# Kernel optimization log

Hardware: AMD Instinct MI355X
Metric: run time of the kernel (lower is better)

Reference implementation:

```python
import jax, jax.numpy as jnp
import numpy as np
from jax import lax

K = 9  # propagation kernel

def conv(x, w, b, pad):
    y = lax.conv_general_dilated(x, w, (1, 1), [(pad, pad), (pad, pad)],
                                 dimension_numbers=('NCHW', 'OIHW', 'NCHW'))
    return y + b[None, :, None, None]

def bn(x, g, beta):
    # SynchronizedBatchNorm2d in eval mode with identity running stats (mean=0, var=1)
    return x * g[None, :, None, None] + beta[None, :, None, None]

def propagate(deep, wts):
    # Dynamic local filtering (same math as img2col * weights, sum over 81 taps),
    # computed as 81 shifted-slice FMAs instead of materializing the (n,c,hw,81) tensor.
    p = K // 2
    n, c, h, w = deep.shape
    padded = jnp.pad(deep, ((0, 0), (0, 0), (p, p), (p, p)))
    out = jnp.zeros_like(deep)
    for k in range(K * K):  # k = dy*9 + dx, matching unfold(2).unfold(3) flattening
        dy, dx = k // K, k % K
        out = out + padded[:, :, dy:dy + h, dx:dx + w] * wts[:, k:k + 1]
    return out

def setup_inputs():
    key = jax.random.key(0)
    ks = jax.random.split(key, 40)
    N, C, H, W = 1, 256, 96, 192
    NUM_CLASSES = 19
    s = 0.05
    f32 = jnp.float32
    d = {}
    d['f1_deep'] = jax.random.normal(ks[0], (N, C, H, W), f32)
    d['f1_low'] = jax.random.normal(ks[1], (N, C, H, W), f32)
    d['f2_low'] = jax.random.normal(ks[2], (N, C, H, W), f32)
    # WeightPredictor
    d['wp_c1_w'] = jax.random.normal(ks[3], (256, 256, 3, 3), f32) * s
    d['wp_c1_b'] = jnp.zeros((256,), f32)
    d['wp_c2_w'] = jax.random.normal(ks[4], (256, 512, 3, 3), f32) * s
    d['wp_c2_b'] = jnp.zeros((256,), f32)
    d['wp_fc_w'] = jax.random.normal(ks[5], (81, 256, 1, 1), f32) * s
    d['wp_fc_b'] = jnp.zeros((81,), f32)
    # AdaptiveScheduler
    d['sch_c1_w'] = jax.random.normal(ks[6], (256, 256, 3, 3), f32) * s
    d['sch_c1_b'] = jnp.zeros((256,), f32)
    d['sch_c2_w'] = jax.random.normal(ks[7], (256, 256, 3, 3), f32) * s
    d['sch_c2_b'] = jnp.zeros((256,), f32)
    d['sch_fc_w'] = jax.random.normal(ks[8], (1, 256), f32) * s
    d['sch_fc_b'] = jnp.zeros((1,), f32)
    # AdaptNet
    d['ad_c1_w'] = jax.random.normal(ks[9], (256, 512, 3, 3), f32) * s
    d['ad_c1_b'] = jnp.zeros((256,), f32)
    d['ad_c2_w'] = jax.random.normal(ks[10], (256, 256, 3, 3), f32) * s
    d['ad_c2_b'] = jnp.zeros((256,), f32)
    d['ad_c3_w'] = jax.random.normal(ks[11], (256, 256, 3, 3), f32) * s
    d['ad_c3_b'] = jnp.zeros((256,), f32)
    # reduce_conv2 (1x1 conv + BN)
    d['rc_w'] = jax.random.normal(ks[12], (48, 256, 1, 1), f32) * s
    d['rc_b'] = jnp.zeros((48,), f32)
    d['rc_g'] = jnp.ones((48,), f32)
    d['rc_beta'] = jnp.zeros((48,), f32)
    # last_conv
    d['lc1_w'] = jax.random.normal(ks[13], (256, 304, 3, 3), f32) * s
    d['lc1_b'] = jnp.zeros((256,), f32)
    d['lc1_g'] = jnp.ones((256,), f32)
    d['lc1_beta'] = jnp.zeros((256,), f32)
    d['lc2_w'] = jax.random.normal(ks[14], (256, 256, 3, 3), f32) * s
    d['lc2_b'] = jnp.zeros((256,), f32)
    d['lc2_g'] = jnp.ones((256,), f32)
    d['lc2_beta'] = jnp.zeros((256,), f32)
    d['lc3_w'] = jax.random.normal(ks[15], (NUM_CLASSES, 256, 1, 1), f32) * s
    d['lc3_b'] = jnp.zeros((NUM_CLASSES,), f32)
    return d

def reference(f1_deep, f1_low, f2_low,
              wp_c1_w, wp_c1_b, wp_c2_w, wp_c2_b, wp_fc_w, wp_fc_b,
              sch_c1_w, sch_c1_b, sch_c2_w, sch_c2_b, sch_fc_w, sch_fc_b,
              ad_c1_w, ad_c1_b, ad_c2_w, ad_c2_b, ad_c3_w, ad_c3_b,
              rc_w, rc_b, rc_g, rc_beta,
              lc1_w, lc1_b, lc1_g, lc1_beta,
              lc2_w, lc2_b, lc2_g, lc2_beta,
              lc3_w, lc3_b):
    n, c, h, w = f1_deep.shape
    # WeightPredictor: shared conv1 applied to both low features, cat, conv2, 1x1, softmax over 81 taps
    a1 = conv(f1_low, wp_c1_w, wp_c1_b, 1)
    a2 = conv(f2_low, wp_c1_w, wp_c1_b, 1)
    f = conv(jnp.concatenate([a1, a2], axis=1), wp_c2_w, wp_c2_b, 1)
    kernel = jax.nn.softmax(conv(f, wp_fc_w, wp_fc_b, 0), axis=1)  # (n,81,h,w)
    # AdaptiveScheduler
    diff = conv(f1_low, sch_c1_w, sch_c1_b, 1) - conv(f2_low, sch_c1_w, sch_c1_b, 1)
    o = conv(diff, sch_c2_w, sch_c2_b, 1)
    pooled = jnp.mean(o, axis=(2, 3)).squeeze()  # (256,) since n=1
    deviation = pooled @ sch_fc_w.T + sch_fc_b  # (1,)
    # PropagationModule (dynamic 9x9 local filtering of f1_deep by predicted per-pixel kernel)
    prop = propagate(f1_deep, kernel)  # (n,256,h,w)
    # AdaptNet
    x = conv(jnp.concatenate([f2_low, prop], axis=1), ad_c1_w, ad_c1_b, 1)
    x = conv(x, ad_c2_w, ad_c2_b, 1)
    x = conv(x, ad_c3_w, ad_c3_b, 1)
    # reduce_conv2 + last_conv
    low = bn(conv(f2_low, rc_w, rc_b, 0), rc_g, rc_beta)  # (n,48,h,w)
    x = jnp.concatenate([x, low], axis=1)  # (n,304,h,w)
    x = bn(conv(x, lc1_w, lc1_b, 1), lc1_g, lc1_beta)
    x = bn(conv(x, lc2_w, lc2_b, 1), lc2_g, lc2_beta)
    x = conv(x, lc3_w, lc3_b, 0)  # (n,19,h,w)
    out = jax.image.resize(x, (x.shape[0], x.shape[1], 4 * h, 4 * w), method='bilinear')
    return (out, deviation)
```

## Files before the change

kernel.cpp:

```cpp
#include <hip/hip_runtime.h>
#include <math.h>

#define HWIMG 18432
#define W2 194
#define H2 98
#define NPX1 (H2 * W2)
#define W4 200
#define H4 104
#define NPX4 (H4 * W4)
#define NOUT (19 * 384 * 768)

typedef short bf16x8 __attribute__((ext_vector_type(8)));
typedef float f32x4 __attribute__((ext_vector_type(4)));

__device__ __forceinline__ ushort bf16r(float f) {
    union { float f; unsigned u; } a; a.f = f;
    unsigned u = a.u;
    return (ushort)((u + 0x7fffu + ((u >> 16) & 1u)) >> 16);
}
__device__ __forceinline__ float b2f(ushort u) {
    union { unsigned i; float f; } a; a.i = ((unsigned)u) << 16;
    return a.f;
}
__device__ __forceinline__ bf16x8 ld8(const ushort* p) {
    return *reinterpret_cast<const bf16x8*>(p);
}

__device__ __forceinline__ void gld16(const ushort* g, ushort* l) {
    __builtin_amdgcn_global_load_lds(
        (const __attribute__((address_space(1))) unsigned int*)g,
        (__attribute__((address_space(3))) unsigned int*)l, 16, 0, 0);
}

#define MF16(a, b, c) __builtin_amdgcn_mfma_f32_16x16x32_bf16(a, b, c, 0, 0, 0)

__device__ __forceinline__ int swz(int L) { return L ^ (((L >> 7) & 7) << 4); }


__global__ __launch_bounds__(256) void xform_t_k(const float* __restrict__ src,
                                                 const float* __restrict__ src2,
                                                 ushort* __restrict__ dst)
{
    const int px = blockIdx.x * 32 + (threadIdx.x & 31);
    const int c8 = (blockIdx.y * 8 + (threadIdx.x >> 5)) * 8;
    if (px >= NPX1) return;
    const int yP = px / W2, xP = px % W2;
    const int y = yP - 1, x = xP - 1;
    ushort v[8];
    if (y >= 0 && y < 96 && x >= 0 && x < 192) {
        const int p = y * 192 + x;
#pragma unroll
        for (int j = 0; j < 8; ++j) {
            float f = src[(size_t)(c8 + j) * HWIMG + p];
            if (src2) f -= src2[(size_t)(c8 + j) * HWIMG + p];
            v[j] = bf16r(f);
        }
    } else {
#pragma unroll
        for (int j = 0; j < 8; ++j) v[j] = 0;
    }
    *reinterpret_cast<uint4*>(dst + ((size_t)(c8 >> 4) * NPX1 + px) * 16 + (c8 & 15))
        = *reinterpret_cast<uint4*>(v);
}

__global__ __launch_bounds__(256) void xform_nhwc_k(const float* __restrict__ src,
                                                    ushort* __restrict__ dst)
{
    const int px = blockIdx.x * 8 + (threadIdx.x >> 5);
    const int c8 = (threadIdx.x & 31) * 8;
    if (px >= NPX4) return;
    const int yP = px / W4, xP = px % W4;
    const int y = yP - 4, x = xP - 4;
    ushort v[8];
    if (y >= 0 && y < 96 && x >= 0 && x < 192) {
        const int p = y * 192 + x;
#pragma unroll
        for (int j = 0; j < 8; ++j) v[j] = bf16r(src[(size_t)(c8 + j) * HWIMG + p]);
    } else {
#pragma unroll
        for (int j = 0; j < 8; ++j) v[j] = 0;
    }
    *reinterpret_cast<uint4*>(dst + (size_t)px * 256 + c8) = *reinterpret_cast<uint4*>(v);
}

__global__ __launch_bounds__(256) void borderzero3_k(ushort* __restrict__ b0,
                                                     ushort* __restrict__ b1,
                                                     ushort* __restrict__ b2)
{
    ushort* buf = (blockIdx.y == 0) ? b0 : ((blockIdx.y == 1) ? b1 : b2);
    const int idx = blockIdx.x * 256 + threadIdx.x;
    if (idx >= 580 * 16) return;
    const int pi = idx % 580;
    const int cb = idx / 580;
    int pp;
    if (pi < 194) pp = pi;
    else if (pi < 388) pp = 97 * 194 + (pi - 194);
    else if (pi < 484) pp = (pi - 388 + 1) * 194;
    else pp = (pi - 484 + 1) * 194 + 193;
    uint4 z = {0, 0, 0, 0};
    ushort* p = buf + ((size_t)cb * NPX1 + pp) * 16;
    *reinterpret_cast<uint4*>(p) = z;
    *reinterpret_cast<uint4*>(p + 8) = z;
}

struct WtxJob {
    const float* w; const float* b; const float* g; const float* beta;
    int CoutR, Coutp, CinR0, kb0e, CinR1, KBt, ntaps, wtoff, biasoff;
};

__global__ __launch_bounds__(256) void wtx_multi_k(WtxJob J0, WtxJob J1, WtxJob J2,
                                                   WtxJob J3, WtxJob J4, WtxJob J5,
                                                   ushort* __restrict__ wt,
                                                   float* __restrict__ biasout)
{
    WtxJob J = J0;
    switch (blockIdx.y) {
        case 1: J = J1; break; case 2: J = J2; break; case 3: J = J3; break;
        case 4: J = J4; break; case 5: J = J5; break; default: break;
    }
    const int idx = blockIdx.x * 256 + threadIdx.x;
    const int total = J.ntaps * J.KBt * J.Coutp * 16;
    const int CinT = J.CinR0 + J.CinR1;
    if (idx < total) {
        const int c16 = idx & 15;
        const int oc = (idx >> 4) % J.Coutp;
        const int r2 = idx / (16 * J.Coutp);
        const int tap = r2 % J.ntaps;
        const int kbt = r2 / J.ntaps;
        const int k = kbt * 16 + c16;
        float val = 0.f;
        if (oc < J.CoutR) {
            int cit = -1;
            if (k < J.kb0e) { if (k < J.CinR0) cit = k; }
            else { const int k1 = k - J.kb0e; if (k1 < J.CinR1) cit = J.CinR0 + k1; }
            if (cit >= 0) {
                val = J.w[((size_t)oc * CinT + cit) * J.ntaps + tap];
                if (J.g) val *= J.g[oc];
            }
        }
        wt[J.wtoff + idx] = bf16r(val);
    } else if (idx < total + J.Coutp) {
        const int oc = idx - total;
        float v = 0.f;
        if (oc < J.CoutR) {
            v = J.b ? J.b[oc] : 0.f;
            if (J.g) v = v * J.g[oc] + J.beta[oc];
        }
        biasout[J.biasoff + oc] = v;
    }
}

struct ConvJob {
    const ushort* in0; const ushort* in1;
    int KB0, KB1;
    const ushort* wt;
    const float* bias;
    ushort* out;
    int CoutWr;
};

template<int NTAPS>
__device__ __forceinline__ void stage_kb(
    const ConvJob& J, int kb, int kbh, char* Ab, char* Bb,
    int y0, int x0, int ocb0, int Coutp, int tid, int b_r, int b_h8, int wu)
{
    constexpr int AROWS = (NTAPS == 9) ? 4 : 2;
    constexpr int AW = (NTAPS == 9) ? 66 : 64;
    constexpr int ASLOTS = AROWS * AW * 2;
    const ushort* plane = (kb < J.KB0)
        ? (J.in0 + (size_t)kb * (NPX1 * 16))
        : (J.in1 + (size_t)(kb - J.KB0) * (NPX1 * 16));
#pragma unroll
    for (int i = 0; i < (ASLOTS + 127) / 128; ++i) {
        const int f16 = i * 128 + tid;
        if ((ASLOTS % 128 == 0) || (f16 < ASLOTS)) {
            const int L = swz(f16 * 16);
            const int e = L >> 5;
            const int h8 = ((L >> 4) & 1) * 8;
            const int r = e / AW;
            const int xx = e - r * AW;
            const int px = (NTAPS == 9)
                ? (y0 - 1 + r) * W2 + (x0 - 1 + xx)
                : (y0 + r) * W2 + (x0 + xx);
            gld16(plane + (size_t)px * 16 + h8,
                  (ushort*)(Ab + __builtin_amdgcn_readfirstlane((f16 & ~63) * 16)));
        }
    }
    const ushort* wsrc = J.wt + ((size_t)kb * NTAPS * Coutp + ocb0 + b_r) * 16 + b_h8;
#pragma unroll
    for (int t = 0; t < NTAPS; ++t) {
        gld16(wsrc + (size_t)t * Coutp * 16, (ushort*)(Bb + (t * 2 + kbh) * 2048 + wu));
    }
}

template<int NTAPS>
__global__ __launch_bounds__(128) void conv_lds_k(ConvJob j0, ConvJob j1, ConvJob j2,
                                                  int Coutp)
{
    constexpr int AROWS = (NTAPS == 9) ? 4 : 2;
    constexpr int AW = (NTAPS == 9) ? 66 : 64;
    constexpr int APLANE = AROWS * AW * 32;
    __shared__ __align__(1024) char Abuf[2 * APLANE];
    __shared__ __align__(1024) char Bbuf[NTAPS * 2 * 2048];

    ConvJob J = j0;
    if (blockIdx.y == 1) J = j1;
    else if (blockIdx.y == 2) J = j2;

    const int nblk = gridDim.x;
    const int cpx = nblk >> 3;
    const int sw = ((int)blockIdx.x & 7) * cpx + ((int)blockIdx.x >> 3);
    const int pt = sw % 144;
    const int ocb0 = (sw / 144) * 64;
    const int y0 = (pt / 3) * 2 + 1;
    const int x0 = (pt % 3) * 64 + 1;

    const int tid = threadIdx.x;
    const int lane = tid & 63;
    const int wm = tid >> 6;
    const int l15 = lane & 15;
    const int kh16 = ((lane >> 4) & 1) * 16;
    const int pl = lane >> 5;

    const int bl = swz(tid * 16);
    const int b_r = bl >> 5;
    const int b_h8 = ((bl >> 4) & 1) * 8;
    const int wu = __builtin_amdgcn_readfirstlane((tid & ~63) * 16);

    const int KBtot = J.KB0 + J.KB1;

    f32x4 acc[4][4] = {};

    for (int s = 0; s < KBtot; s += 2) {
        stage_kb<NTAPS>(J, s,     0, Abuf,          Bbuf, y0, x0, ocb0, Coutp, tid, b_r, b_h8, wu);
        stage_kb<NTAPS>(J, s + 1, 1, Abuf + APLANE, Bbuf, y0, x0, ocb0, Coutp, tid, b_r, b_h8, wu);
        __syncthreads();

        const char* Ap = Abuf + pl * APLANE;
#pragma unroll
        for (int t = 0; t < NTAPS; ++t) {
            const int rowb = (NTAPS == 9) ? ((wm + t / 3) * AW + (t % 3)) : (wm * AW);
            const char* Bp = Bbuf + (t * 2 + pl) * 2048;
            bf16x8 a[4], b[4];
#pragma unroll
            for (int q = 0; q < 4; ++q) {
                const int la = (rowb + q * 16 + l15) * 32 + kh16;
                a[q] = ld8((const ushort*)(Ap + swz(la)));
                const int lb = (q * 16 + l15) * 32 + kh16;
                b[q] = ld8((const ushort*)(Bp + swz(lb)));
            }
#pragma unroll
            for (int i = 0; i < 4; ++i)
#pragma unroll
                for (int j = 0; j < 4; ++j)
                    acc[i][j] = MF16(a[i], b[j], acc[i][j]);
        }
        __syncthreads();
    }

    const int pxbase = (y0 + wm) * W2 + x0;
    const int r4 = (lane >> 4) * 4;
#pragma unroll
    for (int qo = 0; qo < 4; ++qo) {
        if (ocb0 + qo * 16 + 16 > J.CoutWr) continue;
        const int oc = ocb0 + qo * 16 + l15;
        const float bs = J.bias[oc];
        const size_t obase = (size_t)(oc >> 4) * ((size_t)NPX1 * 16) + (oc & 15);
#pragma unroll
        for (int qp = 0; qp < 4; ++qp) {
            const int pp = pxbase + qp * 16 + r4;
#pragma unroll
            for (int r = 0; r < 4; ++r)
                J.out[obase + (size_t)(pp + r) * 16] = bf16r(acc[qp][qo][r] + bs);
        }
    }
}

__global__ __launch_bounds__(256) void softmax81_k(ushort* __restrict__ t)
{
    const int p = blockIdx.x * 256 + threadIdx.x;
    if (p >= HWIMG) return;
    const int y = p / 192, x = p % 192;
    const size_t pp = (size_t)(y + 1) * W2 + (x + 1);
    float v[81];
    float m = -1e30f;
#pragma unroll
    for (int k = 0; k < 81; ++k) {
        v[k] = b2f(t[((size_t)(k >> 4) * NPX1 + pp) * 16 + (k & 15)]);
        m = fmaxf(m, v[k]);
    }
    float s = 0.f;
#pragma unroll
    for (int k = 0; k < 81; ++k) { v[k] = __expf(v[k] - m); s += v[k]; }
    const float inv = 1.f / s;
#pragma unroll
    for (int k = 0; k < 81; ++k)
        t[((size_t)(k >> 4) * NPX1 + pp) * 16 + (k & 15)] = bf16r(v[k] * inv);
}

__global__ __launch_bounds__(256) void prop_k(const ushort* __restrict__ deep,
                                              const ushort* __restrict__ ker,
                                              ushort* __restrict__ out)
{
    __shared__ float kl[8][81];
    const int pxb = blockIdx.x * 8;
    const int t = threadIdx.x;
    for (int i = t; i < 8 * 81; i += 256) {
        const int pp = pxb + i / 81, k = i % 81;
        float kv = 0.f;
        if (pp < NPX1) {
            const int yP = pp / W2, xP = pp % W2;
            if (yP >= 1 && yP <= 96 && xP >= 1 && xP <= 192)
                kv = b2f(ker[((size_t)(k >> 4) * NPX1 + pp) * 16 + (k & 15)]);
        }
        kl[i / 81][k] = kv;
    }
    __syncthreads();
    const int pi = t >> 5;
    const int c8 = (t & 31) * 8;
    const int pp = pxb + pi;
    if (pp >= NPX1) return;
    const int yP = pp / W2, xP = pp % W2;
    ushort* op = out + ((size_t)(c8 >> 4) * NPX1 + pp) * 16 + (c8 & 15);
    if (yP < 1 || yP > 96 || xP < 1 || xP > 192) {
        uint4 z = {0, 0, 0, 0};
        *reinterpret_cast<uint4*>(op) = z;
        return;
    }
    const int y = yP - 1, x = xP - 1;
    float acc[8];
#pragma unroll
    for (int j = 0; j < 8; ++j) acc[j] = 0.f;
    const ushort* dbase = deep + ((size_t)(y + 4) * W4 + (x + 4)) * 256 + c8;
#pragma unroll
    for (int k = 0; k < 81; ++k) {
        const int dy = k / 9 - 4, dx = k % 9 - 4;
        const float kv = kl[pi][k];
        bf16x8 d = ld8(dbase + (ptrdiff_t)(dy * W4 + dx) * 256);
#pragma unroll
        for (int j = 0; j < 8; ++j) acc[j] += b2f((ushort)d[j]) * kv;
    }
    ushort v[8];
#pragma unroll
    for (int j = 0; j < 8; ++j) v[j] = bf16r(acc[j]);
    *reinterpret_cast<uint4*>(op) = *reinterpret_cast<uint4*>(v);
}

__global__ __launch_bounds__(256) void rowsum_k(const ushort* __restrict__ t,
                                                float* __restrict__ partial)
{
    const int y = blockIdx.x >> 2;
    const int bx = blockIdx.x & 3;
    const int c = threadIdx.x;
    const size_t base = ((size_t)(c >> 4) * NPX1 + (size_t)(y + 1) * W2 + 1 + bx * 48) * 16
                      + (c & 15);
    float s = 0.f;
    for (int x = 0; x < 48; ++x) s += b2f(t[base + (size_t)x * 16]);
    partial[(size_t)blockIdx.x * 256 + c] = s;
}

__global__ __launch_bounds__(256) void dev_k(const float* __restrict__ partial,
                                             const float* __restrict__ fcw,
                                             const float* __restrict__ fcb,
                                             float* __restrict__ o)
{
    __shared__ float buf[256];
    const int c = threadIdx.x;
    float s = 0.f;
    for (int i = 0; i < 384; ++i) s += partial[(size_t)i * 256 + c];
    buf[c] = s * fcw[c];
    __syncthreads();
    for (int st = 128; st > 0; st >>= 1) {
        if (c < st) buf[c] += buf[c + st];
        __syncthreads();
    }
    if (c == 0) o[0] = buf[0] * (1.f / (float)HWIMG) + fcb[0];
}

__global__ __launch_bounds__(256) void upsample_k(const ushort* __restrict__ in,
                                                  float* __restrict__ outp)
{
    const int idx = blockIdx.x * 256 + threadIdx.x;
    if (idx >= NOUT) return;
    const int ox = idx % 768;
    const int t = idx / 768;
    const int oy = t % 384;
    const int c = t / 384;

    const float fx = (ox + 0.5f) * 0.25f - 0.5f;
    const float fy = (oy + 0.5f) * 0.25f - 0.5f;
    const int x0 = (int)floorf(fx);
    const int y0 = (int)floorf(fy);
    const float wx = fx - (float)x0;
    const float wy = fy - (float)y0;
    const int x0c = min(max(x0, 0), 191), x1c = min(max(x0 + 1, 0), 191);
    const int y0c = min(max(y0, 0), 95), y1c = min(max(y0 + 1, 0), 95);

    const size_t cb = (size_t)(c >> 4) * NPX1;
    const int c16 = c & 15;
    const float v00 = b2f(in[(cb + (size_t)(y0c + 1) * W2 + (x0c + 1)) * 16 + c16]);
    const float v01 = b2f(in[(cb + (size_t)(y0c + 1) * W2 + (x1c + 1)) * 16 + c16]);
    const float v10 = b2f(in[(cb + (size_t)(y1c + 1) * W2 + (x0c + 1)) * 16 + c16]);
    const float v11 = b2f(in[(cb + (size_t)(y1c + 1) * W2 + (x1c + 1)) * 16 + c16]);
    outp[idx] = (1.f - wy) * ((1.f - wx) * v00 + wx * v01)
              + wy * ((1.f - wx) * v10 + wx * v11);
}

extern "C" void kernel_launch(void* const* d_in, const int* in_sizes, int n_in,
                              void* d_out, int out_size, void* d_ws, size_t ws_size,
                              hipStream_t stream)
{
    const float* f1_deep = (const float*)d_in[0];
    const float* f1_low  = (const float*)d_in[1];
    const float* f2_low  = (const float*)d_in[2];
    const float* wp_c1_w = (const float*)d_in[3];
    const float* wp_c1_b = (const float*)d_in[4];
    const float* wp_c2_w = (const float*)d_in[5];
    const float* wp_c2_b = (const float*)d_in[6];
    const float* wp_fc_w = (const float*)d_in[7];
    const float* wp_fc_b = (const float*)d_in[8];
    const float* sch_c1_w = (const float*)d_in[9];
    const float* sch_c2_w = (const float*)d_in[11];
    const float* sch_c2_b = (const float*)d_in[12];
    const float* sch_fc_w = (const float*)d_in[13];
    const float* sch_fc_b = (const float*)d_in[14];
    const float* ad_c1_w = (const float*)d_in[15];
    const float* ad_c1_b = (const float*)d_in[16];
    const float* ad_c2_w = (const float*)d_in[17];
    const float* ad_c2_b = (const float*)d_in[18];
    const float* ad_c3_w = (const float*)d_in[19];
    const float* ad_c3_b = (const float*)d_in[20];
    const float* rc_w    = (const float*)d_in[21];
    const float* rc_b    = (const float*)d_in[22];
    const float* rc_g    = (const float*)d_in[23];
    const float* rc_beta = (const float*)d_in[24];
    const float* lc1_w   = (const float*)d_in[25];
    const float* lc1_b   = (const float*)d_in[26];
    const float* lc1_g   = (const float*)d_in[27];
    const float* lc1_beta= (const float*)d_in[28];
    const float* lc2_w   = (const float*)d_in[29];
    const float* lc2_b   = (const float*)d_in[30];
    const float* lc2_g   = (const float*)d_in[31];
    const float* lc2_beta= (const float*)d_in[32];
    const float* lc3_w   = (const float*)d_in[33];
    const float* lc3_b   = (const float*)d_in[34];

    float* out = (float*)d_out;
    ushort* ws0 = (ushort*)d_ws;

    const size_t CBBe  = (size_t)NPX1 * 256;
    const size_t BUF0e = (size_t)NPX4 * 256;

    ushort* Bb = ws0 + BUF0e;
    ushort* Cb = Bb + CBBe;
    ushort* Db = Cb + CBBe;
    ushort* Eb = Db + CBBe;
    ushort* Fb = Eb + CBBe;
    ushort* WT = Fb + CBBe;
    float* BIAS = (float*)(WT + 3719168);
    float* PART = (float*)ws0;
    ushort* L48 = Eb + 6 * (size_t)NPX1 * 16;

    const dim3 b256(256), b128(128);

    xform_t_k<<<dim3(595, 4), b256, 0, stream>>>(f1_low, nullptr, Bb);
    xform_t_k<<<dim3(595, 4), b256, 0, stream>>>(f2_low, nullptr, Cb);
    xform_t_k<<<dim3(595, 4), b256, 0, stream>>>(f1_low, f2_low, Db);
    borderzero3_k<<<dim3(37, 3), b256, 0, stream>>>(ws0, Eb, Fb);

    {
        WtxJob w0 = {wp_c1_w, wp_c1_b, nullptr, nullptr, 256, 256, 256, 256, 0, 16, 9, 0, 0};
        WtxJob w1 = {sch_c1_w, nullptr, nullptr, nullptr, 256, 256, 256, 256, 0, 16, 9, 589824, 256};
        WtxJob w2 = {wp_c2_w, wp_c2_b, nullptr, nullptr, 256, 256, 256, 256, 256, 32, 9, 1179648, 512};
        WtxJob w3 = {sch_c2_w, sch_c2_b, nullptr, nullptr, 256, 256, 256, 256, 0, 16, 9, 2359296, 768};
        WtxJob w4 = {wp_fc_w, wp_fc_b, nullptr, nullptr, 81, 128, 256, 256, 0, 16, 1, 2949120, 1024};
        WtxJob w5 = {rc_w, rc_b, rc_g, rc_beta, 48, 128, 256, 256, 0, 16, 1, 2981888, 1280};
        wtx_multi_k<<<dim3(4610, 6), b256, 0, stream>>>(w0, w1, w2, w3, w4, w5, WT, BIAS);
    }

    {
        ConvJob a0 = {Bb, Bb, 16, 0, WT, BIAS, Eb, 256};
        ConvJob a1 = {Cb, Cb, 16, 0, WT, BIAS, Fb, 256};
        ConvJob a2 = {Db, Db, 16, 0, WT + 589824, BIAS + 256, ws0, 256};
        conv_lds_k<9><<<dim3(576, 3), b128, 0, stream>>>(a0, a1, a2, 256);
    }
    {
        ConvJob a0 = {Eb, Fb, 16, 16, WT + 1179648, BIAS + 512, Db, 256};
        ConvJob a1 = {ws0, ws0, 16, 0, WT + 2359296, BIAS + 768, Bb, 256};
        conv_lds_k<9><<<dim3(576, 2), b128, 0, stream>>>(a0, a1, a0, 256);
    }
    rowsum_k<<<384, b256, 0, stream>>>(Bb, PART);
    dev_k<<<1, b256, 0, stream>>>(PART, sch_fc_w, sch_fc_b, out + NOUT);

    {
        ConvJob a0 = {Db, Db, 16, 0, WT + 2949120, BIAS + 1024, Eb, 96};
        ConvJob a1 = {Cb, Cb, 16, 0, WT + 2981888, BIAS + 1280, L48, 64};
        conv_lds_k<1><<<dim3(288, 2), b128, 0, stream>>>(a0, a1, a0, 128);
    }

    {
        WtxJob w0 = {ad_c1_w, ad_c1_b, nullptr, nullptr, 256, 256, 256, 256, 256, 32, 9, 0, 1536};
        WtxJob w1 = {ad_c2_w, ad_c2_b, nullptr, nullptr, 256, 256, 256, 256, 0, 16, 9, 1179648, 1792};
        WtxJob w2 = {ad_c3_w, ad_c3_b, nullptr, nullptr, 256, 256, 256, 256, 0, 16, 9, 1769472, 2048};
        WtxJob w3 = {lc1_w, lc1_b, lc1_g, lc1_beta, 256, 256, 256, 256, 48, 20, 9, 2359296, 2304};
        WtxJob w4 = {lc2_w, lc2_b, lc2_g, lc2_beta, 256, 256, 256, 256, 0, 16, 9, 3096576, 2560};
        WtxJob w5 = {lc3_w, lc3_b, nullptr, nullptr, 19, 128, 256, 256, 0, 16, 1, 3686400, 2816};
        wtx_multi_k<<<dim3(4610, 6), b256, 0, stream>>>(w0, w1, w2, w3, w4, w5, WT, BIAS);
    }

    softmax81_k<<<72, b256, 0, stream>>>(Eb);
    xform_nhwc_k<<<2600, b256, 0, stream>>>(f1_deep, ws0);
    prop_k<<<2377, b256, 0, stream>>>(ws0, Eb, Fb);

    {
        ConvJob a = {Cb, Fb, 16, 16, WT, BIAS + 1536, Bb, 256};
        conv_lds_k<9><<<dim3(576, 1), b128, 0, stream>>>(a, a, a, 256);
    }
    {
        ConvJob a = {Bb, Bb, 16, 0, WT + 1179648, BIAS + 1792, Db, 256};
        conv_lds_k<9><<<dim3(576, 1), b128, 0, stream>>>(a, a, a, 256);
    }
    {
        ConvJob a = {Db, Db, 16, 0, WT + 1769472, BIAS + 2048, Fb, 256};
        conv_lds_k<9><<<dim3(576, 1), b128, 0, stream>>>(a, a, a, 256);
    }
    {
        ConvJob a = {Fb, L48, 16, 4, WT + 2359296, BIAS + 2304, Bb, 256};
        conv_lds_k<9><<<dim3(576, 1), b128, 0, stream>>>(a, a, a, 256);
    }
    {
        ConvJob a = {Bb, Bb, 16, 0, WT + 3096576, BIAS + 2560, Db, 256};
        conv_lds_k<9><<<dim3(576, 1), b128, 0, stream>>>(a, a, a, 256);
    }
    {
        ConvJob a = {Db, Db, 16, 0, WT + 3686400, BIAS + 2816, Cb, 32};
        conv_lds_k<1><<<dim3(288, 1), b128, 0, stream>>>(a, a, a, 128);
    }

    upsample_k<<<(NOUT + 255) / 256, b256, 0, stream>>>(Cb, out);
}
```

Baseline: 498.4 us.

## Double-buffer LDS staging in conv kernel to overlap loads with MFMA compute

Splits the conv main loop into stage and compute helpers and adds a second A/B LDS buffer pair. The next K-step's global-to-LDS loads are issued before computing on the current buffer, with a scheduling barrier between them, so memory latency can hide behind MFMA work. This doubles LDS use per block, which may lower occupancy. The loop also assumes an even number of steps; at the tail it re-stages the last step redundantly.

```diff
diff --git a/kernel.cpp b/kernel.cpp
--- a/kernel.cpp
+++ b/kernel.cpp
@@ -194,14 +194,52 @@
 }
 
 template<int NTAPS>
+__device__ __forceinline__ void stage_step(
+    const ConvJob& J, int st, char* Ab, char* Bb, int APLANE,
+    int y0, int x0, int ocb0, int Coutp, int tid, int b_r, int b_h8, int wu)
+{
+    stage_kb<NTAPS>(J, 2 * st,     0, Ab,          Bb, y0, x0, ocb0, Coutp, tid, b_r, b_h8, wu);
+    stage_kb<NTAPS>(J, 2 * st + 1, 1, Ab + APLANE, Bb, y0, x0, ocb0, Coutp, tid, b_r, b_h8, wu);
+}
+
+template<int NTAPS>
+__device__ __forceinline__ void compute_step(
+    f32x4 acc[4][4], const char* Ab, const char* Bb, int APLANE,
+    int wm, int l15, int kh16, int pl)
+{
+    constexpr int AW = (NTAPS == 9) ? 66 : 64;
+    const char* Ap = Ab + pl * APLANE;
+#pragma unroll
+    for (int t = 0; t < NTAPS; ++t) {
+        const int rowb = (NTAPS == 9) ? ((wm + t / 3) * AW + (t % 3)) : (wm * AW);
+        const char* Bp = Bb + (t * 2 + pl) * 2048;
+        bf16x8 a[4], b[4];
+#pragma unroll
+        for (int q = 0; q < 4; ++q) {
+            const int la = (rowb + q * 16 + l15) * 32 + kh16;
+            a[q] = ld8((const ushort*)(Ap + swz(la)));
+            const int lb = (q * 16 + l15) * 32 + kh16;
+            b[q] = ld8((const ushort*)(Bp + swz(lb)));
+        }
+#pragma unroll
+        for (int i = 0; i < 4; ++i)
+#pragma unroll
+            for (int j = 0; j < 4; ++j)
+                acc[i][j] = MF16(a[i], b[j], acc[i][j]);
+    }
+}
+
+template<int NTAPS>
 __global__ __launch_bounds__(128) void conv_lds_k(ConvJob j0, ConvJob j1, ConvJob j2,
                                                   int Coutp)
 {
     constexpr int AROWS = (NTAPS == 9) ? 4 : 2;
     constexpr int AW = (NTAPS == 9) ? 66 : 64;
     constexpr int APLANE = AROWS * AW * 32;
-    __shared__ __align__(1024) char Abuf[2 * APLANE];
-    __shared__ __align__(1024) char Bbuf[NTAPS * 2 * 2048];
+    __shared__ __align__(1024) char A0[2 * APLANE];
+    __shared__ __align__(1024) char A1[2 * APLANE];
+    __shared__ __align__(1024) char B0[NTAPS * 2 * 2048];
+    __shared__ __align__(1024) char B1[NTAPS * 2 * 2048];
 
     ConvJob J = j0;
     if (blockIdx.y == 1) J = j1;
@@ -228,33 +266,22 @@
     const int wu = __builtin_amdgcn_readfirstlane((tid & ~63) * 16);
 
     const int KBtot = J.KB0 + J.KB1;
+    const int nsteps = KBtot >> 1;
 
     f32x4 acc[4][4] = {};
 
-    for (int s = 0; s < KBtot; s += 2) {
-        stage_kb<NTAPS>(J, s,     0, Abuf,          Bbuf, y0, x0, ocb0, Coutp, tid, b_r, b_h8, wu);
-        stage_kb<NTAPS>(J, s + 1, 1, Abuf + APLANE, Bbuf, y0, x0, ocb0, Coutp, tid, b_r, b_h8, wu);
+    stage_step<NTAPS>(J, 0, A0, B0, APLANE, y0, x0, ocb0, Coutp, tid, b_r, b_h8, wu);
+    __syncthreads();
+
+    for (int s = 0; s < nsteps; s += 2) {
+        stage_step<NTAPS>(J, s + 1, A1, B1, APLANE, y0, x0, ocb0, Coutp, tid, b_r, b_h8, wu);
+        __builtin_amdgcn_sched_barrier(0);
+        compute_step<NTAPS>(acc, A0, B0, APLANE, wm, l15, kh16, pl);
         __syncthreads();
-
-        const char* Ap = Abuf + pl * APLANE;
-#pragma unroll
-        for (int t = 0; t < NTAPS; ++t) {
-            const int rowb = (NTAPS == 9) ? ((wm + t / 3) * AW + (t % 3)) : (wm * AW);
-            const char* Bp = Bbuf + (t * 2 + pl) * 2048;
-            bf16x8 a[4], b[4];
-#pragma unroll
-            for (int q = 0; q < 4; ++q) {
-                const int la = (rowb + q * 16 + l15) * 32 + kh16;
-                a[q] = ld8((const ushort*)(Ap + swz(la)));
-                const int lb = (q * 16 + l15) * 32 + kh16;
-                b[q] = ld8((const ushort*)(Bp + swz(lb)));
-            }
-#pragma unroll
-            for (int i = 0; i < 4; ++i)
-#pragma unroll
-                for (int j = 0; j < 4; ++j)
-                    acc[i][j] = MF16(a[i], b[j], acc[i][j]);
-        }
+        const int sn = (s + 2 < nsteps) ? (s + 2) : (nsteps - 1);
+        stage_step<NTAPS>(J, sn, A0, B0, APLANE, y0, x0, ocb0, Coutp, tid, b_r, b_h8, wu);
+        __builtin_amdgcn_sched_barrier(0);
+        compute_step<NTAPS>(acc, A1, B1, APLANE, wm, l15, kh16, pl);
         __syncthreads();
     }
 
```

Result: slower. 813.7 us (+63.3%).
